# Performance work log

Measured on AMD Instinct MI355X. Metric: run time of the kernel, lower is better.

The kernel has to match this reference:

```python
import jax, jax.numpy as jnp
import numpy as np
from jax.scipy.linalg import expm

N, D, COND_DIM = 1152, 64, 1152
B, T = 16, 1024


def setup_inputs() -> dict:
    key = jax.random.key(0)
    k1, k2, k3, k4, k5 = jax.random.split(key, 5)
    x = jax.random.normal(k1, (B, T, N), dtype=jnp.float32)
    cond = jax.random.normal(k2, (B, COND_DIM), dtype=jnp.float32)
    # learned parameters
    P = jax.random.normal(k3, (N, D), dtype=jnp.float32)
    n_skew = D * (D - 1) // 2
    # nn.Linear default init: U(-1/sqrt(fan_in), 1/sqrt(fan_in))
    bound = 1.0 / np.sqrt(COND_DIM)
    W = jax.random.uniform(k4, (n_skew, COND_DIM), minval=-bound, maxval=bound, dtype=jnp.float32)
    b = jax.random.uniform(k5, (n_skew,), minval=-bound, maxval=bound, dtype=jnp.float32)
    return {"x": x, "cond": cond, "P": P, "W": W, "b": b}


def _rotation(cond, W, b):
    # SiLU -> Linear -> skew-symmetric A -> matrix exponential
    v = jax.nn.silu(cond) @ W.T + b  # (B, D*(D-1)//2)
    iu, ju = jnp.triu_indices(D, k=1)
    A = jnp.zeros((cond.shape[0], D, D), dtype=v.dtype)
    A = A.at[:, iu, ju].set(v).at[:, ju, iu].set(-v)
    return expm(A)  # batched over leading dim, (B, D, D)


def reference(x, cond, P, W, b):
    U, _ = jnp.linalg.qr(P)          # (N, D) orthonormal basis of subspace
    R = _rotation(cond, W, b)        # (B, D, D)
    z = jnp.einsum('btn,nd->btd', x, U)          # project into subspace
    z_rot = jnp.einsum('btd,bde->bte', z, R)     # rotate within subspace
    x_rot = x + jnp.einsum('btd,nd->btn', z_rot - z, U)  # (z_rot - z) @ U.T
    return x_rot
```

## Files before the change

### kernel.cpp

```cpp
#include <hip/hip_runtime.h>
#include <math.h>

#define NN 1152
#define DD 64
#define NSK 2016
#define NB 16
#define NROWS (NB*1024)
#define GPARTS 6
#define KPARTS 6
#define VNBLK 32
#define VBLKS (VNBLK*KPARTS)
#define TBLKS 18

typedef short bf16x8 __attribute__((ext_vector_type(8)));
typedef short bf16x4 __attribute__((ext_vector_type(4)));
typedef float f32x4  __attribute__((ext_vector_type(4)));

__device__ __forceinline__ short bfr(float f){
  unsigned u = __float_as_uint(f);
  u += 0x7fffu + ((u >> 16) & 1u);
  return (short)(u >> 16);
}
__device__ __forceinline__ float htof(short h){
  return __uint_as_float(((unsigned)(unsigned short)h) << 16);
}

__global__ __launch_bounds__(256) void k_pre(const float* __restrict__ cond, const float* __restrict__ W,
                                             float* __restrict__ vpart,
                                             const float* __restrict__ P, float* __restrict__ Gpart,
                                             short* __restrict__ Pbf, short* __restrict__ Ptbf){
  __shared__ float Ps[64*68];
  const int tid = threadIdx.x;
  if (blockIdx.x < VBLKS){
    const int nb = blockIdx.x / KPARTS;
    const int kp = blockIdx.x % KPARTS;
    const int lane = tid & 63, wid = tid >> 6;
    const int m = lane & 15, quad = lane >> 4;
    const int n0 = nb*64 + wid*16;
    if (n0 >= NSK) return;
    f32x4 acc = {0.f,0.f,0.f,0.f};
    const float* crow = &cond[m*NN + kp*192 + quad*8];
    const float* wrow = &W[(n0 + m)*NN + kp*192 + quad*8];
    #pragma unroll
    for (int c = 0; c < 6; ++c){
      const float4 ca = *(const float4*)(crow + c*32);
      const float4 cb = *(const float4*)(crow + c*32 + 4);
      const float4 wa = *(const float4*)(wrow + c*32);
      const float4 wb = *(const float4*)(wrow + c*32 + 4);
      bf16x8 a, b;
      const float cv[8] = {ca.x,ca.y,ca.z,ca.w,cb.x,cb.y,cb.z,cb.w};
      const float wv[8] = {wa.x,wa.y,wa.z,wa.w,wb.x,wb.y,wb.z,wb.w};
      #pragma unroll
      for (int j = 0; j < 8; ++j){
        const float xv = cv[j];
        a[j] = bfr(xv / (1.f + __expf(-xv)));
        b[j] = bfr(wv[j]);
      }
      acc = __builtin_amdgcn_mfma_f32_16x16x32_bf16(a, b, acc, 0, 0, 0);
    }
    #pragma unroll
    for (int r = 0; r < 4; ++r)
      vpart[(kp*16 + quad*4 + r)*NSK + n0 + m] = acc[r];
  } else if (blockIdx.x < VBLKS + GPARTS){
    const int p = blockIdx.x - VBLKS;
    const int lr = tid >> 4, lc = (tid & 15) * 4;
    const int ti = tid >> 4, tj = tid & 15;
    float acc[4][4];
    #pragma unroll
    for (int i=0;i<4;++i){
      #pragma unroll
      for (int j=0;j<4;++j) acc[i][j]=0.f;
    }
    for (int ch = 0; ch < 3; ++ch){
      const int nn0 = p*192 + ch*64;
      __syncthreads();
      #pragma unroll
      for (int ii = 0; ii < 4; ++ii){
        const float4 pv = *(const float4*)&P[(nn0 + lr + 16*ii)*DD + lc];
        *(float4*)&Ps[(lr + 16*ii)*68 + lc] = pv;
      }
      __syncthreads();
      for (int r = 0; r < 64; ++r){
        const float4 a = *(const float4*)&Ps[r*68 + ti*4];
        const float4 b = *(const float4*)&Ps[r*68 + tj*4];
        const float av[4] = {a.x,a.y,a.z,a.w};
        const float bv[4] = {b.x,b.y,b.z,b.w};
        #pragma unroll
        for (int i=0;i<4;++i){
          #pragma unroll
          for (int j=0;j<4;++j) acc[i][j] = fmaf(av[i], bv[j], acc[i][j]);
        }
      }
    }
    float* g = &Gpart[p*DD*DD];
    #pragma unroll
    for (int i=0;i<4;++i){
      float4 ov = make_float4(acc[i][0], acc[i][1], acc[i][2], acc[i][3]);
      *(float4*)&g[(ti*4+i)*DD + tj*4] = ov;
    }
  } else {
    const int t = blockIdx.x - (VBLKS + GPARTS);
    const int n0 = t*64;
    for (int idx = tid; idx < 4096; idx += 256)
      Ps[(idx>>6)*68 + (idx&63)] = P[(n0 + (idx>>6))*DD + (idx&63)];
    __syncthreads();
    for (int idx = tid; idx < 4096; idx += 256){
      const int r = idx>>6, c = idx&63;
      Pbf[(n0+r)*DD + c] = bfr(Ps[r*68 + c]);
    }
    for (int idx = tid; idx < 4096; idx += 256){
      const int d = idx>>6, rr = idx&63;
      Ptbf[d*NN + n0 + rr] = bfr(Ps[rr*68 + d]);
    }
  }
}

__device__ __forceinline__ void mmul68(const float* __restrict__ A, const float* __restrict__ B,
                                       float* __restrict__ C, int tid){
  __syncthreads();
  const int w = tid >> 6, lane = tid & 63;
  const int r0 = (w & 3) * 16 + (lane >> 3) * 2;
  const int c0 = (w >> 2) * 32 + (lane & 7) * 4;
  float acc[2][4];
  #pragma unroll
  for (int i=0;i<2;++i){
    #pragma unroll
    for (int j=0;j<4;++j) acc[i][j]=0.f;
  }
  for (int kq = 0; kq < 16; ++kq){
    float4 b[4];
    #pragma unroll
    for (int kk=0;kk<4;++kk) b[kk] = *(const float4*)&B[(kq*4+kk)*68 + c0];
    const float4 a0 = *(const float4*)&A[(r0    )*68 + kq*4];
    const float4 a1 = *(const float4*)&A[(r0 + 1)*68 + kq*4];
    const float av0[4] = {a0.x,a0.y,a0.z,a0.w};
    const float av1[4] = {a1.x,a1.y,a1.z,a1.w};
    #pragma unroll
    for (int kk=0;kk<4;++kk){
      acc[0][0] = fmaf(av0[kk], b[kk].x, acc[0][0]);
      acc[0][1] = fmaf(av0[kk], b[kk].y, acc[0][1]);
      acc[0][2] = fmaf(av0[kk], b[kk].z, acc[0][2]);
      acc[0][3] = fmaf(av0[kk], b[kk].w, acc[0][3]);
      acc[1][0] = fmaf(av1[kk], b[kk].x, acc[1][0]);
      acc[1][1] = fmaf(av1[kk], b[kk].y, acc[1][1]);
      acc[1][2] = fmaf(av1[kk], b[kk].z, acc[1][2]);
      acc[1][3] = fmaf(av1[kk], b[kk].w, acc[1][3]);
    }
  }
  *(float4*)&C[(r0    )*68 + c0] = make_float4(acc[0][0],acc[0][1],acc[0][2],acc[0][3]);
  *(float4*)&C[(r0 + 1)*68 + c0] = make_float4(acc[1][0],acc[1][1],acc[1][2],acc[1][3]);
  __syncthreads();
}

__global__ __launch_bounds__(512,1) void k_fused(const float* __restrict__ Gpart, const float* __restrict__ P,
                                                 const float* __restrict__ vpart, const float* __restrict__ bias,
                                                 float* __restrict__ Mg, float* __restrict__ Rinvg,
                                                 const float* __restrict__ x, const short* __restrict__ Ptbf,
                                                 short* __restrict__ ybf){
  __shared__ float Bs[64*68], B2[64*68], B3[64*68], Tb[64*68], Xb[64*68];
  __shared__ float red[512];
  __shared__ float scl_s;
  __shared__ int   ssh_s;
  const int tid = threadIdx.x;
  if (blockIdx.x > NB){
    const int lane = tid & 63, wid = tid >> 6;
    const int row0 = (blockIdx.x - NB - 1) * 64;
    const int m    = lane & 15, quad = lane >> 4;
    const int r0 = (wid & 3) * 16;
    const int c0 = (wid >> 2) * 32;
    f32x4 acc0 = {0.f,0.f,0.f,0.f}, acc1 = {0.f,0.f,0.f,0.f};
    const float* xrow = &x[(row0 + r0 + m)*NN + quad*8];
    const short* ut0  = &Ptbf[(c0      + m)*NN + quad*8];
    const short* ut1  = &Ptbf[(c0 + 16 + m)*NN + quad*8];
    float4 xa = *(const float4*)(xrow);
    float4 xb = *(const float4*)(xrow + 4);
    bf16x8 b0 = *(const bf16x8*)(ut0);
    bf16x8 b1 = *(const bf16x8*)(ut1);
    for (int kc = 0; kc < NN; kc += 32){
      float4 nxa, nxb; bf16x8 nb0, nb1;
      if (kc + 32 < NN){
        nxa = *(const float4*)(xrow + kc + 32);
        nxb = *(const float4*)(xrow + kc + 36);
        nb0 = *(const bf16x8*)(ut0 + kc + 32);
        nb1 = *(const bf16x8*)(ut1 + kc + 32);
      }
      bf16x8 a;
      a[0]=bfr(xa.x); a[1]=bfr(xa.y); a[2]=bfr(xa.z); a[3]=bfr(xa.w);
      a[4]=bfr(xb.x); a[5]=bfr(xb.y); a[6]=bfr(xb.z); a[7]=bfr(xb.w);
      acc0 = __builtin_amdgcn_mfma_f32_16x16x32_bf16(a, b0, acc0, 0, 0, 0);
      acc1 = __builtin_amdgcn_mfma_f32_16x16x32_bf16(a, b1, acc1, 0, 0, 0);
      xa = nxa; xb = nxb; b0 = nb0; b1 = nb1;
    }
    #pragma unroll
    for (int q = 0; q < 4; ++q){
      ybf[(row0 + r0 + quad*4 + q)*DD + c0      + m] = bfr(acc0[q]);
      ybf[(row0 + r0 + quad*4 + q)*DD + c0 + 16 + m] = bfr(acc1[q]);
    }
    return;
  }
  if (blockIdx.x == NB){
    if (tid < 64){
      const int j = tid;
      float Gc[DD], Wc[DD], Rc[DD];
      #pragma unroll
      for (int i = 0; i < DD; ++i){
        float g = 0.f;
        #pragma unroll
        for (int p = 0; p < GPARTS; ++p) g += Gpart[p*4096 + i*DD + j];
        Gc[i] = g;
        Wc[i] = P[i*DD + j];
      }
      #pragma unroll
      for (int k = 0; k < DD; ++k){
        const float gkk = __shfl(Gc[k], k);
        const float wkk = __shfl(Wc[k], k);
        const float beta = (wkk >= 0.f) ? -sqrtf(gkk) : sqrtf(gkk);
        const float wkj = Wc[k];
        const float dj  = Gc[k] - beta*wkj;
        const float cj  = dj / (beta*(beta - wkk));
        float rkj = wkj + dj/beta;
        if (j == k) rkj = beta;
        if (j <  k) rkj = 0.f;
        Rc[k] = rkj;
        #pragma unroll
        for (int i = k+1; i < DD; ++i){
          const float wik = __shfl(Wc[i], k);
          const float rki = __shfl(rkj, i);
          Wc[i] = fmaf(-cj,  wik, Wc[i]);
          Gc[i] = fmaf(-rki, rkj, Gc[i]);
        }
      }
      #pragma unroll
      for (int i = 0; i < DD; ++i) Bs[i*68 + j] = Rc[i];
    }
    __syncthreads();
    if (tid < 64){
      const int j = tid;
      float Xc[DD];
      #pragma unroll
      for (int i = DD-1; i >= 0; --i){
        float acc = (i==j) ? 1.f : 0.f;
        #pragma unroll
        for (int l = i+1; l < DD; ++l)
          acc = fmaf(-Bs[i*68 + l], Xc[l], acc);
        Xc[i] = acc / Bs[i*68 + i];
      }
      #pragma unroll
      for (int i = 0; i < DD; ++i)
        Rinvg[i*DD + j] = Xc[i];
    }
    return;
  }
  const int b = blockIdx.x;
  for (int idx = tid; idx < 64*64; idx += 512)
    Xb[(idx>>6)*68 + (idx&63)] = 0.f;
  __syncthreads();
  for (int idx = tid; idx < NSK; idx += 512){
    int i = (int)((127.0f - sqrtf(16129.0f - 8.0f*(float)idx)) * 0.5f);
    while (i*(127 - i)/2 > idx) --i;
    while ((i+1)*(127 - (i+1))/2 <= idx) ++i;
    const int jj = idx - i*(127 - i)/2 + i + 1;
    float val = bias[idx];
    #pragma unroll
    for (int p = 0; p < KPARTS; ++p) val += vpart[(p*16 + b)*NSK + idx];
    Xb[i*68 + jj] = val;
    Xb[jj*68 + i] = -val;
  }
  __syncthreads();
  {
    const int c = tid & 63, g = tid >> 6;
    float s = 0.f;
    for (int r = g*8; r < g*8 + 8; ++r) s += fabsf(Xb[r*68 + c]);
    red[g*64 + c] = s;
    __syncthreads();
    if (tid < 64){
      float cs = 0.f;
      #pragma unroll
      for (int g2 = 0; g2 < 8; ++g2) cs += red[g2*64 + tid];
      #pragma unroll
      for (int off = 32; off > 0; off >>= 1) cs = fmaxf(cs, __shfl_xor(cs, off));
      if (tid == 0){
        int s2 = 0; float scale = 1.f;
        float nrm = cs;
        while (nrm > 1.0f && s2 < 40){ nrm *= 0.5f; scale *= 0.5f; ++s2; }
        ssh_s = s2; scl_s = scale;
      }
    }
    __syncthreads();
  }
  const float scale = scl_s;
  const int   sq    = ssh_s;
  for (int idx = tid; idx < 64*64; idx += 512){
    const int i = idx>>6, jj = idx&63;
    Bs[i*68 + jj] = Xb[i*68 + jj] * scale;
  }
  mmul68(Bs, Bs, B2, tid);
  mmul68(B2, Bs, B3, tid);
  for (int idx = tid; idx < 64*64; idx += 512){
    const int i = idx>>6, jj = idx&63;
    const int o = i*68 + jj;
    Tb[o] = (i==jj ? (1.f/720.f) : 0.f) + Bs[o]*(1.f/5040.f) + B2[o]*(1.f/40320.f) + B3[o]*(1.f/362880.f);
  }
  mmul68(B3, Tb, Xb, tid);
  for (int idx = tid; idx < 64*64; idx += 512){
    const int i = idx>>6, jj = idx&63;
    const int o = i*68 + jj;
    Xb[o] += (i==jj ? (1.f/6.f) : 0.f) + Bs[o]*(1.f/24.f) + B2[o]*(1.f/120.f);
  }
  mmul68(B3, Xb, Tb, tid);
  for (int idx = tid; idx < 64*64; idx += 512){
    const int i = idx>>6, jj = idx&63;
    const int o = i*68 + jj;
    Tb[o] += (i==jj ? 1.f : 0.f) + Bs[o] + B2[o]*0.5f;
  }
  float* cur = Tb;
  float* oth = Xb;
  for (int r = 0; r < sq; ++r){
    mmul68(cur, cur, oth, tid);
    float* t = cur; cur = oth; oth = t;
  }
  for (int idx = tid; idx < 64*64; idx += 512){
    const int i = idx>>6, jj = idx&63;
    Mg[b*4096 + idx] = cur[i*68 + jj] - (i==jj ? 1.f : 0.f);
  }
}

__global__ __launch_bounds__(256) void k_kmat(const float* __restrict__ Rinvg, const float* __restrict__ Mg,
                                              float* __restrict__ Kg){
  __shared__ float Ri[64*68], Ms[64*68], Ts[64*68];
  const int b = blockIdx.x, tid = threadIdx.x;
  for (int idx = tid; idx < 4096; idx += 256){
    const int r = idx>>6, c = idx&63;
    Ri[r*68 + c] = Rinvg[idx];
    Ms[r*68 + c] = Mg[b*4096 + idx];
  }
  __syncthreads();
  const int ti = tid >> 4, tj = tid & 15;
  {
    float acc[4][4];
    #pragma unroll
    for (int i=0;i<4;++i){
      #pragma unroll
      for (int j=0;j<4;++j) acc[i][j]=0.f;
    }
    for (int kq = 0; kq < 16; ++kq){
      float4 a[4], bm[4];
      #pragma unroll
      for (int i=0;i<4;++i) a[i] = *(const float4*)&Ri[(ti*4+i)*68 + kq*4];
      #pragma unroll
      for (int kk=0;kk<4;++kk) bm[kk] = *(const float4*)&Ms[(kq*4+kk)*68 + tj*4];
      #pragma unroll
      for (int i=0;i<4;++i){
        const float av[4] = {a[i].x,a[i].y,a[i].z,a[i].w};
        #pragma unroll
        for (int kk=0;kk<4;++kk){
          acc[i][0] = fmaf(av[kk], bm[kk].x, acc[i][0]);
          acc[i][1] = fmaf(av[kk], bm[kk].y, acc[i][1]);
          acc[i][2] = fmaf(av[kk], bm[kk].z, acc[i][2]);
          acc[i][3] = fmaf(av[kk], bm[kk].w, acc[i][3]);
        }
      }
    }
    __syncthreads();
    #pragma unroll
    for (int i=0;i<4;++i)
      *(float4*)&Ts[(ti*4+i)*68 + tj*4] = make_float4(acc[i][0],acc[i][1],acc[i][2],acc[i][3]);
    __syncthreads();
  }
  {
    float acc[4][4];
    #pragma unroll
    for (int i=0;i<4;++i){
      #pragma unroll
      for (int j=0;j<4;++j) acc[i][j]=0.f;
    }
    for (int kq = 0; kq < 16; ++kq){
      float4 a[4], bt[4];
      #pragma unroll
      for (int i=0;i<4;++i) a[i] = *(const float4*)&Ts[(ti*4+i)*68 + kq*4];
      #pragma unroll
      for (int j=0;j<4;++j) bt[j] = *(const float4*)&Ri[(tj*4+j)*68 + kq*4];
      #pragma unroll
      for (int i=0;i<4;++i){
        #pragma unroll
        for (int j=0;j<4;++j){
          acc[i][j] = fmaf(a[i].x, bt[j].x, acc[i][j]);
          acc[i][j] = fmaf(a[i].y, bt[j].y, acc[i][j]);
          acc[i][j] = fmaf(a[i].z, bt[j].z, acc[i][j]);
          acc[i][j] = fmaf(a[i].w, bt[j].w, acc[i][j]);
        }
      }
    }
    #pragma unroll
    for (int i=0;i<4;++i)
      *(float4*)&Kg[b*4096 + (ti*4+i)*DD + tj*4] = make_float4(acc[i][0],acc[i][1],acc[i][2],acc[i][3]);
  }
}

__global__ __launch_bounds__(256) void k_wout(const float* __restrict__ x, const short* __restrict__ Pbf,
                                              const short* __restrict__ ybf, const float* __restrict__ Kg,
                                              float* __restrict__ out){
  __shared__ float Ks[64*68];
  __shared__ float ys[16*68];
  __shared__ short wbf[16*72];
  const int tid  = threadIdx.x;
  const int lane = tid & 63, wid = tid >> 6;
  const int row0 = blockIdx.x * 16;
  const int bb   = row0 >> 10;
  const int m    = lane & 15, quad = lane >> 4;
  for (int idx = tid; idx < 4096; idx += 256)
    Ks[(idx>>6)*68 + (idx&63)] = Kg[bb*4096 + idx];
  {
    const int idx = tid*4;
    const int r = idx >> 6, c = idx & 63;
    bf16x4 yv = *(const bf16x4*)&ybf[(row0 + r)*DD + c];
    ys[r*68 + c    ] = htof(yv[0]);
    ys[r*68 + c + 1] = htof(yv[1]);
    ys[r*68 + c + 2] = htof(yv[2]);
    ys[r*68 + c + 3] = htof(yv[3]);
  }
  __syncthreads();
  {
    const int r = tid >> 4, c4 = (tid & 15)*4;
    float w0[4] = {0.f,0.f,0.f,0.f};
    for (int k = 0; k < 64; ++k){
      const float yr = ys[r*68 + k];
      const float4 kv = *(const float4*)&Ks[k*68 + c4];
      w0[0] = fmaf(yr, kv.x, w0[0]);
      w0[1] = fmaf(yr, kv.y, w0[1]);
      w0[2] = fmaf(yr, kv.z, w0[2]);
      w0[3] = fmaf(yr, kv.w, w0[3]);
    }
    bf16x4 pk;
    #pragma unroll
    for (int jj = 0; jj < 4; ++jj) pk[jj] = bfr(w0[jj]);
    *(bf16x4*)&wbf[r*72 + c4] = pk;
  }
  __syncthreads();
  const int q4 = quad * 4;
  bf16x8 wa0 = *(const bf16x8*)&wbf[m*72 +      quad*8];
  bf16x8 wa1 = *(const bf16x8*)&wbf[m*72 + 32 + quad*8];
  bf16x8 ub0 = *(const bf16x8*)&Pbf[(wid*16 + m)*DD +      quad*8];
  bf16x8 ub1 = *(const bf16x8*)&Pbf[(wid*16 + m)*DD + 32 + quad*8];
  float xq0 = x[(row0 + q4 + 0)*NN + wid*16 + m];
  float xq1 = x[(row0 + q4 + 1)*NN + wid*16 + m];
  float xq2 = x[(row0 + q4 + 2)*NN + wid*16 + m];
  float xq3 = x[(row0 + q4 + 3)*NN + wid*16 + m];
  for (int it = 0; it < 18; ++it){
    const int n0 = (wid + 4*it) * 16;
    f32x4 acc = {0.f,0.f,0.f,0.f};
    acc = __builtin_amdgcn_mfma_f32_16x16x32_bf16(wa0, ub0, acc, 0, 0, 0);
    acc = __builtin_amdgcn_mfma_f32_16x16x32_bf16(wa1, ub1, acc, 0, 0, 0);
    const float o0 = xq0 + acc[0];
    const float o1 = xq1 + acc[1];
    const float o2 = xq2 + acc[2];
    const float o3 = xq3 + acc[3];
    if (it < 17){
      const int n1 = n0 + 64;
      ub0 = *(const bf16x8*)&Pbf[(n1 + m)*DD +      quad*8];
      ub1 = *(const bf16x8*)&Pbf[(n1 + m)*DD + 32 + quad*8];
      xq0 = x[(row0 + q4 + 0)*NN + n1 + m];
      xq1 = x[(row0 + q4 + 1)*NN + n1 + m];
      xq2 = x[(row0 + q4 + 2)*NN + n1 + m];
      xq3 = x[(row0 + q4 + 3)*NN + n1 + m];
    }
    out[(row0 + q4 + 0)*NN + n0 + m] = o0;
    out[(row0 + q4 + 1)*NN + n0 + m] = o1;
    out[(row0 + q4 + 2)*NN + n0 + m] = o2;
    out[(row0 + q4 + 3)*NN + n0 + m] = o3;
  }
}

extern "C" void kernel_launch(void* const* d_in, const int* in_sizes, int n_in,
                              void* d_out, int out_size, void* d_ws, size_t ws_size,
                              hipStream_t stream) {
  const float* x    = (const float*)d_in[0];
  const float* cond = (const float*)d_in[1];
  const float* P    = (const float*)d_in[2];
  const float* W    = (const float*)d_in[3];
  const float* bias = (const float*)d_in[4];
  float* out = (float*)d_out;
  float* ws  = (float*)d_ws;

  float* Gpart = ws;
  float* vpart = ws + 24576;
  float* Kg    = ws + 24576;
  float* Mg    = ws + 218112;
  float* Rinvg = ws + 283648;
  short* Pbf   = (short*)(ws + 287744);
  short* Ptbf  = (short*)(ws + 324608);
  short* ybf   = (short*)(ws + 361472);

  hipLaunchKernelGGL(k_pre,  dim3(VBLKS + GPARTS + TBLKS), dim3(256), 0, stream,
                     cond, W, vpart, P, Gpart, Pbf, Ptbf);
  hipLaunchKernelGGL(k_fused, dim3(NB + 1 + NROWS/64), dim3(512), 0, stream,
                     Gpart, P, vpart, bias, Mg, Rinvg, x, Ptbf, ybf);
  hipLaunchKernelGGL(k_kmat, dim3(NB), dim3(256), 0, stream, Rinvg, Mg, Kg);
  hipLaunchKernelGGL(k_wout, dim3(NROWS/16), dim3(256), 0, stream, x, Pbf, ybf, Kg, out);
}
```

Measured before the change: 241.2 us.

## Stage output tile through LDS for float4 coalesced x/out access; prefetch mmul68 operands

In the output kernel, MFMA results are written to a double-buffered shared-memory tile, then each thread reads x and writes out as float4 rows, replacing scalar strided 4-byte accesses. This targets the memory-bound residual-add and store over the large x/out tensors. It adds a barrier per iteration and drops the previous register prefetch of x and P. Separately, the 64x64 LDS matmul helper now software-prefetches the next k-slice of A and B into registers.

```diff
diff --git a/kernel.cpp b/kernel.cpp
--- a/kernel.cpp
+++ b/kernel.cpp
@@ -10,6 +10,7 @@
 #define KPARTS 6
 #define VNBLK 32
 #define VBLKS (VNBLK*KPARTS)
+#define TOFF (VBLKS + GPARTS)
 #define TBLKS 18
 
 typedef short bf16x8 __attribute__((ext_vector_type(8)));
@@ -61,7 +62,7 @@
     #pragma unroll
     for (int r = 0; r < 4; ++r)
       vpart[(kp*16 + quad*4 + r)*NSK + n0 + m] = acc[r];
-  } else if (blockIdx.x < VBLKS + GPARTS){
+  } else if (blockIdx.x < TOFF){
     const int p = blockIdx.x - VBLKS;
     const int lr = tid >> 4, lc = (tid & 15) * 4;
     const int ti = tid >> 4, tj = tid & 15;
@@ -99,7 +100,7 @@
       *(float4*)&g[(ti*4+i)*DD + tj*4] = ov;
     }
   } else {
-    const int t = blockIdx.x - (VBLKS + GPARTS);
+    const int t = blockIdx.x - TOFF;
     const int n0 = t*64;
     for (int idx = tid; idx < 4096; idx += 256)
       Ps[(idx>>6)*68 + (idx&63)] = P[(n0 + (idx>>6))*DD + (idx&63)];
@@ -127,25 +128,38 @@
     #pragma unroll
     for (int j=0;j<4;++j) acc[i][j]=0.f;
   }
+  float4 b0 = *(const float4*)&B[0*68 + c0];
+  float4 b1 = *(const float4*)&B[1*68 + c0];
+  float4 b2 = *(const float4*)&B[2*68 + c0];
+  float4 b3 = *(const float4*)&B[3*68 + c0];
+  float4 a0 = *(const float4*)&A[(r0    )*68];
+  float4 a1 = *(const float4*)&A[(r0 + 1)*68];
   for (int kq = 0; kq < 16; ++kq){
-    float4 b[4];
-    #pragma unroll
-    for (int kk=0;kk<4;++kk) b[kk] = *(const float4*)&B[(kq*4+kk)*68 + c0];
-    const float4 a0 = *(const float4*)&A[(r0    )*68 + kq*4];
-    const float4 a1 = *(const float4*)&A[(r0 + 1)*68 + kq*4];
+    float4 nb0, nb1, nb2, nb3, na0, na1;
+    if (kq < 15){
+      const int k4 = (kq+1)*4;
+      nb0 = *(const float4*)&B[(k4+0)*68 + c0];
+      nb1 = *(const float4*)&B[(k4+1)*68 + c0];
+      nb2 = *(const float4*)&B[(k4+2)*68 + c0];
+      nb3 = *(const float4*)&B[(k4+3)*68 + c0];
+      na0 = *(const float4*)&A[(r0    )*68 + k4];
+      na1 = *(const float4*)&A[(r0 + 1)*68 + k4];
+    }
     const float av0[4] = {a0.x,a0.y,a0.z,a0.w};
     const float av1[4] = {a1.x,a1.y,a1.z,a1.w};
+    const float4 bb[4] = {b0,b1,b2,b3};
     #pragma unroll
     for (int kk=0;kk<4;++kk){
-      acc[0][0] = fmaf(av0[kk], b[kk].x, acc[0][0]);
-      acc[0][1] = fmaf(av0[kk], b[kk].y, acc[0][1]);
-      acc[0][2] = fmaf(av0[kk], b[kk].z, acc[0][2]);
-      acc[0][3] = fmaf(av0[kk], b[kk].w, acc[0][3]);
-      acc[1][0] = fmaf(av1[kk], b[kk].x, acc[1][0]);
-      acc[1][1] = fmaf(av1[kk], b[kk].y, acc[1][1]);
-      acc[1][2] = fmaf(av1[kk], b[kk].z, acc[1][2]);
-      acc[1][3] = fmaf(av1[kk], b[kk].w, acc[1][3]);
-    }
+      acc[0][0] = fmaf(av0[kk], bb[kk].x, acc[0][0]);
+      acc[0][1] = fmaf(av0[kk], bb[kk].y, acc[0][1]);
+      acc[0][2] = fmaf(av0[kk], bb[kk].z, acc[0][2]);
+      acc[0][3] = fmaf(av0[kk], bb[kk].w, acc[0][3]);
+      acc[1][0] = fmaf(av1[kk], bb[kk].x, acc[1][0]);
+      acc[1][1] = fmaf(av1[kk], bb[kk].y, acc[1][1]);
+      acc[1][2] = fmaf(av1[kk], bb[kk].z, acc[1][2]);
+      acc[1][3] = fmaf(av1[kk], bb[kk].w, acc[1][3]);
+    }
+    b0 = nb0; b1 = nb1; b2 = nb2; b3 = nb3; a0 = na0; a1 = na1;
   }
   *(float4*)&C[(r0    )*68 + c0] = make_float4(acc[0][0],acc[0][1],acc[0][2],acc[0][3]);
   *(float4*)&C[(r0 + 1)*68 + c0] = make_float4(acc[1][0],acc[1][1],acc[1][2],acc[1][3]);
@@ -403,6 +417,7 @@
   __shared__ float Ks[64*68];
   __shared__ float ys[16*68];
   __shared__ short wbf[16*72];
+  __shared__ float os[2][16*68];
   const int tid  = threadIdx.x;
   const int lane = tid & 63, wid = tid >> 6;
   const int row0 = blockIdx.x * 16;
@@ -437,37 +452,26 @@
     *(bf16x4*)&wbf[r*72 + c4] = pk;
   }
   __syncthreads();
-  const int q4 = quad * 4;
   bf16x8 wa0 = *(const bf16x8*)&wbf[m*72 +      quad*8];
   bf16x8 wa1 = *(const bf16x8*)&wbf[m*72 + 32 + quad*8];
-  bf16x8 ub0 = *(const bf16x8*)&Pbf[(wid*16 + m)*DD +      quad*8];
-  bf16x8 ub1 = *(const bf16x8*)&Pbf[(wid*16 + m)*DD + 32 + quad*8];
-  float xq0 = x[(row0 + q4 + 0)*NN + wid*16 + m];
-  float xq1 = x[(row0 + q4 + 1)*NN + wid*16 + m];
-  float xq2 = x[(row0 + q4 + 2)*NN + wid*16 + m];
-  float xq3 = x[(row0 + q4 + 3)*NN + wid*16 + m];
+  const int er = tid >> 4;
+  const int ec = (tid & 15) * 4;
   for (int it = 0; it < 18; ++it){
-    const int n0 = (wid + 4*it) * 16;
+    const int n0 = it*64 + wid*16;
+    bf16x8 ub0 = *(const bf16x8*)&Pbf[(n0 + m)*DD +      quad*8];
+    bf16x8 ub1 = *(const bf16x8*)&Pbf[(n0 + m)*DD + 32 + quad*8];
     f32x4 acc = {0.f,0.f,0.f,0.f};
     acc = __builtin_amdgcn_mfma_f32_16x16x32_bf16(wa0, ub0, acc, 0, 0, 0);
     acc = __builtin_amdgcn_mfma_f32_16x16x32_bf16(wa1, ub1, acc, 0, 0, 0);
-    const float o0 = xq0 + acc[0];
-    const float o1 = xq1 + acc[1];
-    const float o2 = xq2 + acc[2];
-    const float o3 = xq3 + acc[3];
-    if (it < 17){
-      const int n1 = n0 + 64;
-      ub0 = *(const bf16x8*)&Pbf[(n1 + m)*DD +      quad*8];
-      ub1 = *(const bf16x8*)&Pbf[(n1 + m)*DD + 32 + quad*8];
-      xq0 = x[(row0 + q4 + 0)*NN + n1 + m];
-      xq1 = x[(row0 + q4 + 1)*NN + n1 + m];
-      xq2 = x[(row0 + q4 + 2)*NN + n1 + m];
-      xq3 = x[(row0 + q4 + 3)*NN + n1 + m];
-    }
-    out[(row0 + q4 + 0)*NN + n0 + m] = o0;
-    out[(row0 + q4 + 1)*NN + n0 + m] = o1;
-    out[(row0 + q4 + 2)*NN + n0 + m] = o2;
-    out[(row0 + q4 + 3)*NN + n0 + m] = o3;
+    float* ob = os[it & 1];
+    #pragma unroll
+    for (int q = 0; q < 4; ++q)
+      ob[(quad*4 + q)*68 + wid*16 + m] = acc[q];
+    __syncthreads();
+    const float4 xv = *(const float4*)&x[(row0 + er)*NN + it*64 + ec];
+    const float4 ov = *(const float4*)&ob[er*68 + ec];
+    *(float4*)&out[(row0 + er)*NN + it*64 + ec] =
+        make_float4(xv.x + ov.x, xv.y + ov.y, xv.z + ov.z, xv.w + ov.w);
   }
 }
 
```

New measurement: 239.9 us. No clear change (-0.5%).

## Fuse projection, rotation and write-back into one per-row-tile kernel

Applied to the files above, without the earlier changes.

Removes the separate K-matrix kernel and the bf16 y round trip through global memory. Each 64-row block now computes its projection in-block, applies Rinv, M and Rinv^T with shared-memory FP32 matmuls, and writes the output through a double-buffered shared staging tile with coalesced float4 stores. The projection no longer overlaps the matrix-exponential blocks, which now run as their own small kernel first. Each row block also redoes the 64x64 matmuls and uses a large shared-memory footprint, which limits occupancy to one block.

```diff
diff --git a/kernel.cpp b/kernel.cpp
--- a/kernel.cpp
+++ b/kernel.cpp
@@ -10,6 +10,7 @@
 #define KPARTS 6
 #define VNBLK 32
 #define VBLKS (VNBLK*KPARTS)
+#define TOFF (VBLKS + GPARTS)
 #define TBLKS 18
 
 typedef short bf16x8 __attribute__((ext_vector_type(8)));
@@ -61,7 +62,7 @@
     #pragma unroll
     for (int r = 0; r < 4; ++r)
       vpart[(kp*16 + quad*4 + r)*NSK + n0 + m] = acc[r];
-  } else if (blockIdx.x < VBLKS + GPARTS){
+  } else if (blockIdx.x < TOFF){
     const int p = blockIdx.x - VBLKS;
     const int lr = tid >> 4, lc = (tid & 15) * 4;
     const int ti = tid >> 4, tj = tid & 15;
@@ -99,7 +100,7 @@
       *(float4*)&g[(ti*4+i)*DD + tj*4] = ov;
     }
   } else {
-    const int t = blockIdx.x - (VBLKS + GPARTS);
+    const int t = blockIdx.x - TOFF;
     const int n0 = t*64;
     for (int idx = tid; idx < 4096; idx += 256)
       Ps[(idx>>6)*68 + (idx&63)] = P[(n0 + (idx>>6))*DD + (idx&63)];
@@ -152,52 +153,54 @@
   __syncthreads();
 }
 
-__global__ __launch_bounds__(512,1) void k_fused(const float* __restrict__ Gpart, const float* __restrict__ P,
-                                                 const float* __restrict__ vpart, const float* __restrict__ bias,
-                                                 float* __restrict__ Mg, float* __restrict__ Rinvg,
-                                                 const float* __restrict__ x, const short* __restrict__ Ptbf,
-                                                 short* __restrict__ ybf){
+__device__ __forceinline__ void mmul68_w(const float* __restrict__ A, const float* __restrict__ B,
+                                         short* __restrict__ Wb, int tid){
+  __syncthreads();
+  const int w = tid >> 6, lane = tid & 63;
+  const int r0 = (w & 3) * 16 + (lane >> 3) * 2;
+  const int c0 = (w >> 2) * 32 + (lane & 7) * 4;
+  float acc[2][4];
+  #pragma unroll
+  for (int i=0;i<2;++i){
+    #pragma unroll
+    for (int j=0;j<4;++j) acc[i][j]=0.f;
+  }
+  for (int kq = 0; kq < 16; ++kq){
+    float4 b[4];
+    #pragma unroll
+    for (int kk=0;kk<4;++kk) b[kk] = *(const float4*)&B[(kq*4+kk)*68 + c0];
+    const float4 a0 = *(const float4*)&A[(r0    )*68 + kq*4];
+    const float4 a1 = *(const float4*)&A[(r0 + 1)*68 + kq*4];
+    const float av0[4] = {a0.x,a0.y,a0.z,a0.w};
+    const float av1[4] = {a1.x,a1.y,a1.z,a1.w};
+    #pragma unroll
+    for (int kk=0;kk<4;++kk){
+      acc[0][0] = fmaf(av0[kk], b[kk].x, acc[0][0]);
+      acc[0][1] = fmaf(av0[kk], b[kk].y, acc[0][1]);
+      acc[0][2] = fmaf(av0[kk], b[kk].z, acc[0][2]);
+      acc[0][3] = fmaf(av0[kk], b[kk].w, acc[0][3]);
+      acc[1][0] = fmaf(av1[kk], b[kk].x, acc[1][0]);
+      acc[1][1] = fmaf(av1[kk], b[kk].y, acc[1][1]);
+      acc[1][2] = fmaf(av1[kk], b[kk].z, acc[1][2]);
+      acc[1][3] = fmaf(av1[kk], b[kk].w, acc[1][3]);
+    }
+  }
+  bf16x4 p0, p1;
+  #pragma unroll
+  for (int j=0;j<4;++j){ p0[j] = bfr(acc[0][j]); p1[j] = bfr(acc[1][j]); }
+  *(bf16x4*)&Wb[(r0    )*72 + c0] = p0;
+  *(bf16x4*)&Wb[(r0 + 1)*72 + c0] = p1;
+  __syncthreads();
+}
+
+__global__ __launch_bounds__(512,1) void k_exp(const float* __restrict__ Gpart, const float* __restrict__ P,
+                                               const float* __restrict__ vpart, const float* __restrict__ bias,
+                                               float* __restrict__ Mg, float* __restrict__ Rinvg){
   __shared__ float Bs[64*68], B2[64*68], B3[64*68], Tb[64*68], Xb[64*68];
   __shared__ float red[512];
   __shared__ float scl_s;
   __shared__ int   ssh_s;
   const int tid = threadIdx.x;
-  if (blockIdx.x > NB){
-    const int lane = tid & 63, wid = tid >> 6;
-    const int row0 = (blockIdx.x - NB - 1) * 64;
-    const int m    = lane & 15, quad = lane >> 4;
-    const int r0 = (wid & 3) * 16;
-    const int c0 = (wid >> 2) * 32;
-    f32x4 acc0 = {0.f,0.f,0.f,0.f}, acc1 = {0.f,0.f,0.f,0.f};
-    const float* xrow = &x[(row0 + r0 + m)*NN + quad*8];
-    const short* ut0  = &Ptbf[(c0      + m)*NN + quad*8];
-    const short* ut1  = &Ptbf[(c0 + 16 + m)*NN + quad*8];
-    float4 xa = *(const float4*)(xrow);
-    float4 xb = *(const float4*)(xrow + 4);
-    bf16x8 b0 = *(const bf16x8*)(ut0);
-    bf16x8 b1 = *(const bf16x8*)(ut1);
-    for (int kc = 0; kc < NN; kc += 32){
-      float4 nxa, nxb; bf16x8 nb0, nb1;
-      if (kc + 32 < NN){
-        nxa = *(const float4*)(xrow + kc + 32);
-        nxb = *(const float4*)(xrow + kc + 36);
-        nb0 = *(const bf16x8*)(ut0 + kc + 32);
-        nb1 = *(const bf16x8*)(ut1 + kc + 32);
-      }
-      bf16x8 a;
-      a[0]=bfr(xa.x); a[1]=bfr(xa.y); a[2]=bfr(xa.z); a[3]=bfr(xa.w);
-      a[4]=bfr(xb.x); a[5]=bfr(xb.y); a[6]=bfr(xb.z); a[7]=bfr(xb.w);
-      acc0 = __builtin_amdgcn_mfma_f32_16x16x32_bf16(a, b0, acc0, 0, 0, 0);
-      acc1 = __builtin_amdgcn_mfma_f32_16x16x32_bf16(a, b1, acc1, 0, 0, 0);
-      xa = nxa; xb = nxb; b0 = nb0; b1 = nb1;
-    }
-    #pragma unroll
-    for (int q = 0; q < 4; ++q){
-      ybf[(row0 + r0 + quad*4 + q)*DD + c0      + m] = bfr(acc0[q]);
-      ybf[(row0 + r0 + quad*4 + q)*DD + c0 + 16 + m] = bfr(acc1[q]);
-    }
-    return;
-  }
   if (blockIdx.x == NB){
     if (tid < 64){
       const int j = tid;
@@ -325,149 +328,92 @@
   }
 }
 
-__global__ __launch_bounds__(256) void k_kmat(const float* __restrict__ Rinvg, const float* __restrict__ Mg,
-                                              float* __restrict__ Kg){
-  __shared__ float Ri[64*68], Ms[64*68], Ts[64*68];
-  const int b = blockIdx.x, tid = threadIdx.x;
-  for (int idx = tid; idx < 4096; idx += 256){
-    const int r = idx>>6, c = idx&63;
-    Ri[r*68 + c] = Rinvg[idx];
-    Ms[r*68 + c] = Mg[b*4096 + idx];
-  }
-  __syncthreads();
-  const int ti = tid >> 4, tj = tid & 15;
-  {
-    float acc[4][4];
-    #pragma unroll
-    for (int i=0;i<4;++i){
-      #pragma unroll
-      for (int j=0;j<4;++j) acc[i][j]=0.f;
-    }
-    for (int kq = 0; kq < 16; ++kq){
-      float4 a[4], bm[4];
-      #pragma unroll
-      for (int i=0;i<4;++i) a[i] = *(const float4*)&Ri[(ti*4+i)*68 + kq*4];
-      #pragma unroll
-      for (int kk=0;kk<4;++kk) bm[kk] = *(const float4*)&Ms[(kq*4+kk)*68 + tj*4];
-      #pragma unroll
-      for (int i=0;i<4;++i){
-        const float av[4] = {a[i].x,a[i].y,a[i].z,a[i].w};
-        #pragma unroll
-        for (int kk=0;kk<4;++kk){
-          acc[i][0] = fmaf(av[kk], bm[kk].x, acc[i][0]);
-          acc[i][1] = fmaf(av[kk], bm[kk].y, acc[i][1]);
-          acc[i][2] = fmaf(av[kk], bm[kk].z, acc[i][2]);
-          acc[i][3] = fmaf(av[kk], bm[kk].w, acc[i][3]);
-        }
-      }
-    }
-    __syncthreads();
-    #pragma unroll
-    for (int i=0;i<4;++i)
-      *(float4*)&Ts[(ti*4+i)*68 + tj*4] = make_float4(acc[i][0],acc[i][1],acc[i][2],acc[i][3]);
-    __syncthreads();
-  }
-  {
-    float acc[4][4];
-    #pragma unroll
-    for (int i=0;i<4;++i){
-      #pragma unroll
-      for (int j=0;j<4;++j) acc[i][j]=0.f;
-    }
-    for (int kq = 0; kq < 16; ++kq){
-      float4 a[4], bt[4];
-      #pragma unroll
-      for (int i=0;i<4;++i) a[i] = *(const float4*)&Ts[(ti*4+i)*68 + kq*4];
-      #pragma unroll
-      for (int j=0;j<4;++j) bt[j] = *(const float4*)&Ri[(tj*4+j)*68 + kq*4];
-      #pragma unroll
-      for (int i=0;i<4;++i){
-        #pragma unroll
-        for (int j=0;j<4;++j){
-          acc[i][j] = fmaf(a[i].x, bt[j].x, acc[i][j]);
-          acc[i][j] = fmaf(a[i].y, bt[j].y, acc[i][j]);
-          acc[i][j] = fmaf(a[i].z, bt[j].z, acc[i][j]);
-          acc[i][j] = fmaf(a[i].w, bt[j].w, acc[i][j]);
-        }
-      }
-    }
-    #pragma unroll
-    for (int i=0;i<4;++i)
-      *(float4*)&Kg[b*4096 + (ti*4+i)*DD + tj*4] = make_float4(acc[i][0],acc[i][1],acc[i][2],acc[i][3]);
-  }
-}
-
-__global__ __launch_bounds__(256) void k_wout(const float* __restrict__ x, const short* __restrict__ Pbf,
-                                              const short* __restrict__ ybf, const float* __restrict__ Kg,
-                                              float* __restrict__ out){
-  __shared__ float Ks[64*68];
-  __shared__ float ys[16*68];
-  __shared__ short wbf[16*72];
+__global__ __launch_bounds__(512,1) void k_all(const float* __restrict__ x, const short* __restrict__ Ptbf,
+                                               const short* __restrict__ Pbf, const float* __restrict__ Mg,
+                                               const float* __restrict__ Rinvg, float* __restrict__ out){
+  __shared__ float zs[64*68], ts[64*68];
+  __shared__ float Ri[64*68], Ric[64*68], Ms[64*68];
+  __shared__ short wbf[64*72];
+  __shared__ float os[2][64*68];
   const int tid  = threadIdx.x;
   const int lane = tid & 63, wid = tid >> 6;
-  const int row0 = blockIdx.x * 16;
-  const int bb   = row0 >> 10;
+  const int row0 = blockIdx.x * 64;
+  const int bb   = blockIdx.x >> 4;
   const int m    = lane & 15, quad = lane >> 4;
-  for (int idx = tid; idx < 4096; idx += 256)
-    Ks[(idx>>6)*68 + (idx&63)] = Kg[bb*4096 + idx];
+
+  for (int idx = tid; idx < 4096; idx += 512){
+    const int r = idx>>6, c = idx&63;
+    Ri [r*68 + c] = Rinvg[r*DD + c];
+    Ric[r*68 + c] = Rinvg[c*DD + r];
+    Ms [r*68 + c] = Mg[bb*4096 + idx];
+  }
+
   {
-    const int idx = tid*4;
-    const int r = idx >> 6, c = idx & 63;
-    bf16x4 yv = *(const bf16x4*)&ybf[(row0 + r)*DD + c];
-    ys[r*68 + c    ] = htof(yv[0]);
-    ys[r*68 + c + 1] = htof(yv[1]);
-    ys[r*68 + c + 2] = htof(yv[2]);
-    ys[r*68 + c + 3] = htof(yv[3]);
-  }
-  __syncthreads();
-  {
-    const int r = tid >> 4, c4 = (tid & 15)*4;
-    float w0[4] = {0.f,0.f,0.f,0.f};
-    for (int k = 0; k < 64; ++k){
-      const float yr = ys[r*68 + k];
-      const float4 kv = *(const float4*)&Ks[k*68 + c4];
-      w0[0] = fmaf(yr, kv.x, w0[0]);
-      w0[1] = fmaf(yr, kv.y, w0[1]);
-      w0[2] = fmaf(yr, kv.z, w0[2]);
-      w0[3] = fmaf(yr, kv.w, w0[3]);
-    }
-    bf16x4 pk;
-    #pragma unroll
-    for (int jj = 0; jj < 4; ++jj) pk[jj] = bfr(w0[jj]);
-    *(bf16x4*)&wbf[r*72 + c4] = pk;
-  }
-  __syncthreads();
-  const int q4 = quad * 4;
-  bf16x8 wa0 = *(const bf16x8*)&wbf[m*72 +      quad*8];
-  bf16x8 wa1 = *(const bf16x8*)&wbf[m*72 + 32 + quad*8];
-  bf16x8 ub0 = *(const bf16x8*)&Pbf[(wid*16 + m)*DD +      quad*8];
-  bf16x8 ub1 = *(const bf16x8*)&Pbf[(wid*16 + m)*DD + 32 + quad*8];
-  float xq0 = x[(row0 + q4 + 0)*NN + wid*16 + m];
-  float xq1 = x[(row0 + q4 + 1)*NN + wid*16 + m];
-  float xq2 = x[(row0 + q4 + 2)*NN + wid*16 + m];
-  float xq3 = x[(row0 + q4 + 3)*NN + wid*16 + m];
+    const int r0 = (wid & 3) * 16;
+    const int c0 = (wid >> 2) * 32;
+    f32x4 acc0 = {0.f,0.f,0.f,0.f}, acc1 = {0.f,0.f,0.f,0.f};
+    const float* xrow = &x[(row0 + r0 + m)*NN + quad*8];
+    const short* ut0  = &Ptbf[(c0      + m)*NN + quad*8];
+    const short* ut1  = &Ptbf[(c0 + 16 + m)*NN + quad*8];
+    float4 xa = *(const float4*)(xrow);
+    float4 xb = *(const float4*)(xrow + 4);
+    bf16x8 b0 = *(const bf16x8*)(ut0);
+    bf16x8 b1 = *(const bf16x8*)(ut1);
+    for (int kc = 0; kc < NN; kc += 32){
+      float4 nxa, nxb; bf16x8 nb0, nb1;
+      if (kc + 32 < NN){
+        nxa = *(const float4*)(xrow + kc + 32);
+        nxb = *(const float4*)(xrow + kc + 36);
+        nb0 = *(const bf16x8*)(ut0 + kc + 32);
+        nb1 = *(const bf16x8*)(ut1 + kc + 32);
+      }
+      bf16x8 a;
+      a[0]=bfr(xa.x); a[1]=bfr(xa.y); a[2]=bfr(xa.z); a[3]=bfr(xa.w);
+      a[4]=bfr(xb.x); a[5]=bfr(xb.y); a[6]=bfr(xb.z); a[7]=bfr(xb.w);
+      acc0 = __builtin_amdgcn_mfma_f32_16x16x32_bf16(a, b0, acc0, 0, 0, 0);
+      acc1 = __builtin_amdgcn_mfma_f32_16x16x32_bf16(a, b1, acc1, 0, 0, 0);
+      xa = nxa; xb = nxb; b0 = nb0; b1 = nb1;
+    }
+    #pragma unroll
+    for (int q = 0; q < 4; ++q){
+      zs[(r0 + quad*4 + q)*68 + c0      + m] = acc0[q];
+      zs[(r0 + quad*4 + q)*68 + c0 + 16 + m] = acc1[q];
+    }
+  }
+
+  mmul68  (zs, Ri,  ts, tid);
+  mmul68  (ts, Ms,  zs, tid);
+  mmul68_w(zs, Ric, wbf, tid);
+
+  const int rt  = wid & 3;
+  const int ctA = wid >> 2;
+  bf16x8 wa0 = *(const bf16x8*)&wbf[(rt*16 + m)*72 +      quad*8];
+  bf16x8 wa1 = *(const bf16x8*)&wbf[(rt*16 + m)*72 + 32 + quad*8];
   for (int it = 0; it < 18; ++it){
-    const int n0 = (wid + 4*it) * 16;
-    f32x4 acc = {0.f,0.f,0.f,0.f};
-    acc = __builtin_amdgcn_mfma_f32_16x16x32_bf16(wa0, ub0, acc, 0, 0, 0);
-    acc = __builtin_amdgcn_mfma_f32_16x16x32_bf16(wa1, ub1, acc, 0, 0, 0);
-    const float o0 = xq0 + acc[0];
-    const float o1 = xq1 + acc[1];
-    const float o2 = xq2 + acc[2];
-    const float o3 = xq3 + acc[3];
-    if (it < 17){
-      const int n1 = n0 + 64;
-      ub0 = *(const bf16x8*)&Pbf[(n1 + m)*DD +      quad*8];
-      ub1 = *(const bf16x8*)&Pbf[(n1 + m)*DD + 32 + quad*8];
-      xq0 = x[(row0 + q4 + 0)*NN + n1 + m];
-      xq1 = x[(row0 + q4 + 1)*NN + n1 + m];
-      xq2 = x[(row0 + q4 + 2)*NN + n1 + m];
-      xq3 = x[(row0 + q4 + 3)*NN + n1 + m];
-    }
-    out[(row0 + q4 + 0)*NN + n0 + m] = o0;
-    out[(row0 + q4 + 1)*NN + n0 + m] = o1;
-    out[(row0 + q4 + 2)*NN + n0 + m] = o2;
-    out[(row0 + q4 + 3)*NN + n0 + m] = o3;
+    float* ob = os[it & 1];
+    #pragma unroll
+    for (int half = 0; half < 2; ++half){
+      const int ct  = ctA + half*2;
+      const int n0c = it*64 + ct*16;
+      const bf16x8 ub0 = *(const bf16x8*)&Pbf[(n0c + m)*DD +      quad*8];
+      const bf16x8 ub1 = *(const bf16x8*)&Pbf[(n0c + m)*DD + 32 + quad*8];
+      f32x4 acc = {0.f,0.f,0.f,0.f};
+      acc = __builtin_amdgcn_mfma_f32_16x16x32_bf16(wa0, ub0, acc, 0, 0, 0);
+      acc = __builtin_amdgcn_mfma_f32_16x16x32_bf16(wa1, ub1, acc, 0, 0, 0);
+      #pragma unroll
+      for (int q = 0; q < 4; ++q)
+        ob[(rt*16 + quad*4 + q)*68 + ct*16 + m] = acc[q];
+    }
+    __syncthreads();
+    #pragma unroll
+    for (int p = 0; p < 2; ++p){
+      const int idx = tid + p*512;
+      const int er = idx >> 4, ec = (idx & 15) * 4;
+      const float4 xv = *(const float4*)&x[(row0 + er)*NN + it*64 + ec];
+      const float4 ov = *(const float4*)&ob[er*68 + ec];
+      *(float4*)&out[(row0 + er)*NN + it*64 + ec] =
+          make_float4(xv.x + ov.x, xv.y + ov.y, xv.z + ov.z, xv.w + ov.w);
+    }
   }
 }
 
@@ -484,17 +430,15 @@
 
   float* Gpart = ws;
   float* vpart = ws + 24576;
-  float* Kg    = ws + 24576;
   float* Mg    = ws + 218112;
   float* Rinvg = ws + 283648;
   short* Pbf   = (short*)(ws + 287744);
   short* Ptbf  = (short*)(ws + 324608);
-  short* ybf   = (short*)(ws + 361472);
-
-  hipLaunchKernelGGL(k_pre,  dim3(VBLKS + GPARTS + TBLKS), dim3(256), 0, stream,
+
+  hipLaunchKernelGGL(k_pre, dim3(VBLKS + GPARTS + TBLKS), dim3(256), 0, stream,
                      cond, W, vpart, P, Gpart, Pbf, Ptbf);
-  hipLaunchKernelGGL(k_fused, dim3(NB + 1 + NROWS/64), dim3(512), 0, stream,
-                     Gpart, P, vpart, bias, Mg, Rinvg, x, Ptbf, ybf);
-  hipLaunchKernelGGL(k_kmat, dim3(NB), dim3(256), 0, stream, Rinvg, Mg, Kg);
-  hipLaunchKernelGGL(k_wout, dim3(NROWS/16), dim3(256), 0, stream, x, Pbf, ybf, Kg, out);
-}
+  hipLaunchKernelGGL(k_exp, dim3(NB + 1), dim3(512), 0, stream,
+                     Gpart, P, vpart, bias, Mg, Rinvg);
+  hipLaunchKernelGGL(k_all, dim3(NROWS/64), dim3(512), 0, stream,
+                     x, Ptbf, Pbf, Mg, Rinvg, out);
+}
```

Result: slower. 596.5 us (+147.4%).
